# Performance work log

Hardware: AMD Instinct MI355X
Metric: run time of the kernel (lower is better)

## Reference

```python
import jax, jax.numpy as jnp
import numpy as np
from math import comb

N_DERIV = 4          # num_derivatives
ODE_DIM = 512        # ode_dimension
K = ODE_DIM * (N_DERIV + 1)


def _build_system(n, d):
    # system_matrices_1d: A_1d = flip(pascal), Q_1d = flip(hilbert), chol(Q_1d)
    x = np.arange(n + 1)
    B = np.array([[comb(i, j) for j in range(n + 1)] for i in range(n + 1)], dtype=np.float64)
    A1 = B[::-1, ::-1]                                  # flip both axes
    Hil = 1.0 / (x[:, None] + x[None, :] + 1.0)
    Q1 = Hil[::-1, ::-1]
    L1 = np.linalg.cholesky(Q1)
    a = np.kron(np.eye(d), A1)
    q = np.kron(np.eye(d), L1)
    return jnp.asarray(a, jnp.float32), jnp.asarray(q, jnp.float32)


def _qr_r(x):
    # sqrtm_to_cholesky: upper-triangular factor from reduced QR
    return jnp.linalg.qr(x)[1]


def setup_inputs() -> dict:
    key = jax.random.key(0)
    k1, k2, k3, k4, k5 = jax.random.split(key, 5)
    a, q_sqrtm_lower = _build_system(N_DERIV, ODE_DIM)
    m0 = jax.random.normal(k1, (K,), dtype=jnp.float32)
    l0 = jnp.tril(jax.random.normal(k2, (K, K), dtype=jnp.float32) * 0.05)
    H = jax.random.normal(k3, (ODE_DIM, K), dtype=jnp.float32) * 0.1
    bias = jax.random.normal(k4, (ODE_DIM,), dtype=jnp.float32)
    dt = jax.random.uniform(k5, (1,), dtype=jnp.float32, minval=0.05, maxval=0.15)
    return {"m0": m0, "l0": l0, "H": H, "bias": bias, "dt": dt,
            "a": a, "q_sqrtm_lower": q_sqrtm_lower}


def reference(m0, l0, H, bias, dt, a, q_sqrtm_lower):
    d = H.shape[0]
    k = m0.shape[0]
    n1 = k // d                       # num_derivatives + 1
    # --- assemble_preconditioner ---
    powers = jnp.arange(n1 - 1, -1, -1, dtype=m0.dtype)
    scales = jnp.exp(jax.lax.lgamma(powers + 1.0))
    pw = powers + 0.5
    adt = jnp.abs(dt[0])
    p = jnp.tile(adt ** pw / scales, d)          # (k,)
    p_inv = jnp.tile(adt ** (-pw) * scales, d)   # (k,)
    # --- extrapolate_mean ---
    m0_p = p_inv * m0
    m_ext_p = a @ m0_p
    m_ext = p * m_ext_p
    # EK-style linearized observation residual
    m_obs = H @ m_ext - bias                     # (d,)
    # --- estimate_error ---
    l_obs_ns_e = H @ (p_inv[:, None] * q_sqrtm_lower)            # (d,k)
    l_obs_raw = _qr_r(l_obs_ns_e.T).T                            # lower (d,d)
    res_white = jax.scipy.linalg.solve_triangular(l_obs_raw.T, m_obs, lower=False)
    diffusion = jnp.sqrt(jnp.dot(res_white, res_white) / res_white.size)
    error = diffusion * jnp.sqrt(jnp.einsum('nj,nj->n', l_obs_raw, l_obs_raw))
    # --- complete_extrapolation (sum_of_sqrtm_factors) ---
    R1 = (a @ (p_inv[:, None] * l0)).T           # (k,k)
    R2 = (diffusion * q_sqrtm_lower).T           # (k,k)
    l_ext_p = _qr_r(jnp.vstack([R1, R2])).T      # lower (k,k)
    l_ext = p[:, None] * l_ext_p
    # --- final_correction ---
    l_obs_ns = H @ l_ext                         # (d,k)
    l_obs = _qr_r(l_obs_ns.T).T                  # lower (d,d)
    crosscov = l_ext @ l_obs_ns.T                # (k,d)
    gain = jax.scipy.linalg.cho_solve((l_obs, True), crosscov.T).T  # (k,d)
    m_cor = m_ext - gain @ m_obs
    l_cor = l_ext - gain @ l_obs_ns
    u = jnp.reshape(m_cor, (-1, d), order='F')[0]  # derivative-0 block
    return m_cor, l_cor, u, error, diffusion
```

## Files before the change

kernel.cpp:

```cpp
#include <hip/hip_runtime.h>
#include <math.h>

#define KDIM 2560
#define DDIM 512
#define NB 64

#define QM 2560
#define QM2 1024
#define QN 512
#define PW 16
#define UW 4

#define OUT_LCOR 2560
#define OUT_U    6556160
#define OUT_ERR  6556672
#define OUT_DIFF 6557184


__global__ void k_setup(const float* dt, double* scal){
  if (threadIdx.x==0 && blockIdx.x==0){
    double adt = fabs((double)dt[0]);
    const double scales[5] = {24.0,6.0,2.0,1.0,1.0};
    for (int i=0;i<5;i++){
      double pw = (double)(4-i)+0.5;
      scal[i]   = pow(adt, pw)/scales[i];
      scal[5+i] = pow(adt,-pw)*scales[i];
    }
  }
}

__global__ __launch_bounds__(256) void k_mext_mobs(const float* a, const float* m0, const float* H,
                                                   const float* bias, const double* scal,
                                                   double* mext, double* mobs){
  __shared__ double me[KDIM];
  __shared__ double red[256];
  double pp[5], pv[5];
  #pragma unroll
  for (int i=0;i<5;i++){ pp[i]=scal[i]; pv[i]=scal[5+i]; }
  int tid=threadIdx.x;
  for (int r=tid; r<KDIM; r+=256){
    int j=r/5, i=r%5;
    const float* arow = a + (size_t)r*KDIM + 5*j;
    const float* m0b  = m0 + 5*j;
    double acc=0;
    #pragma unroll
    for (int l=0;l<5;l++) acc += (double)arow[l]*pv[l]*(double)m0b[l];
    me[r] = pp[i]*acc;
  }
  __syncthreads();
  if (blockIdx.x==0) for (int r=tid;r<KDIM;r+=256) mext[r]=me[r];
  int b = blockIdx.x;
  const float* Hr = H + (size_t)b*KDIM;
  double acc=0;
  for (int c=tid;c<KDIM;c+=256) acc += (double)Hr[c]*me[c];
  red[tid]=acc; __syncthreads();
  for (int s=128;s>0;s>>=1){ if (tid<s) red[tid]+=red[tid+s]; __syncthreads(); }
  if (tid==0) mobs[b] = red[0] - (double)bias[b];
}

__global__ void k_A2(const float* H, const float* q, const double* scal,
                     double* Atop, double* Abot){
  int idx = blockIdx.x*blockDim.x+threadIdx.x;
  if (idx >= QN*QM) return;
  double pv[5];
  #pragma unroll
  for (int t=0;t<5;t++) pv[t]=scal[5+t];
  int j = idx / QM;
  int i = idx % QM;
  int bi = i/5;
  double acc=0;
  #pragma unroll
  for (int t=0;t<5;t++)
    acc += (double)H[(size_t)j*QM + 5*bi+t]*pv[t]*(double)q[(size_t)(5*bi+t)*QM + i];
  if (i < 512) Atop[(size_t)j*QM2 + i] = acc;
  else         Abot[(size_t)j*2048 + (i-512)] = acc;
}

__global__ void k_copyB(const double* Gbot, double* AQ){
  int idx = blockIdx.x*blockDim.x+threadIdx.x;
  if (idx >= 512*512) return;
  int c = idx/512, rr = idx%512;
  AQ[(size_t)c*QM2 + 512 + rr] = (rr<=c) ? Gbot[(size_t)c*512 + rr] : 0.0;
}

__global__ __launch_bounds__(1024) void qr_panel(double* A, double* vhead, int col0, double* Tbuf){
  __shared__ double redw[16][PW];
  __shared__ double rednorm[16];
  __shared__ double sh[3];
  __shared__ double wsh[PW];
  __shared__ double alphas[PW], betas[PW];
  __shared__ double VtVs[PW][PW];
  __shared__ double Tsh[PW][PW];
  int tid=threadIdx.x, wid=tid>>6, lane=tid&63;
  int m = QM2 - col0;
  bool on = tid < m;
  double x[PW];
  #pragma unroll
  for (int j=0;j<PW;j++)
    x[j] = on ? A[(size_t)(col0+j)*QM2 + col0 + tid] : 0.0;
  for (int j=0;j<PW;j++){
    double v0 = (tid>=j && on)? x[j] : 0.0;
    double ps = v0*v0;
    #pragma unroll
    for (int o=32;o>0;o>>=1) ps += __shfl_down(ps,o);
    if (lane==0) rednorm[wid]=ps;
    if (tid==j) sh[0]=x[j];
    __syncthreads();
    if (tid==0){
      double s0=0;
      for (int t=0;t<16;t++) s0+=rednorm[t];
      double x1=sh[0];
      double nrm=sqrt(s0);
      double alpha=(x1>=0.0)?-nrm:nrm;
      double v1=x1-alpha;
      double vtv=s0-2.0*alpha*x1+alpha*alpha;
      double b=(vtv>0.0)?2.0/vtv:0.0;
      sh[1]=v1; sh[2]=b;
      alphas[j]=alpha; betas[j]=b;
      vhead[col0+j]=v1;
    }
    __syncthreads();
    if (tid==j) x[j]=sh[1];
    double b=sh[2];
    double v=(tid>=j && on)? x[j] : 0.0;
    #pragma unroll
    for (int t=0;t<PW;t++){
      if (t==j) continue;
      double p=v*x[t];
      #pragma unroll
      for (int o=32;o>0;o>>=1) p+=__shfl_down(p,o);
      if (lane==0) redw[wid][t]=p;
    }
    __syncthreads();
    if (tid<PW && tid!=j){
      double tot=0;
      #pragma unroll
      for (int t2=0;t2<16;t2++) tot+=redw[t2][tid];
      if (tid>j) wsh[tid]=b*tot;
      else       VtVs[tid][j]=tot;
    }
    __syncthreads();
    if (v!=0.0){
      for (int t=j+1;t<PW;t++) x[t]-=wsh[t]*v;
    }
  }
  __syncthreads();
  if (tid<PW){
    int i=tid;
    Tsh[i][i]=betas[i];
    for (int j2=i+1;j2<PW;j2++){
      double z=0;
      for (int t=i;t<j2;t++) z+=Tsh[i][t]*VtVs[t][j2];
      Tsh[i][j2]=-betas[j2]*z;
    }
  }
  __syncthreads();
  for (int e=tid;e<PW*PW;e+=1024){
    int i=e/PW, j2=e%PW;
    Tbuf[e] = (j2>=i)? Tsh[i][j2] : 0.0;
  }
  if (on){
    #pragma unroll
    for (int j=0;j<PW;j++)
      A[(size_t)(col0+j)*QM2 + col0 + tid] = (tid==j)? alphas[j] : x[j];
  }
}

__global__ __launch_bounds__(256) void qr_update(double* A, const double* vhead,
                                                 const double* Tbuf, int col0){
  __shared__ double redu[4][PW];
  __shared__ double ysh[PW];
  __shared__ double wsh[PW];
  int tid=threadIdx.x, wid=tid>>6, lane=tid&63;
  int cc=col0+PW+blockIdx.x;
  int m=QM2-col0;
  double a[UW];
  #pragma unroll
  for (int w=0;w<UW;w++){
    int lr=tid+w*256;
    a[w]=(lr<m)? A[(size_t)cc*QM2+col0+lr] : 0.0;
  }
  double acc[PW];
  #pragma unroll
  for (int j=0;j<PW;j++) acc[j]=0;
  #pragma unroll
  for (int w=0;w<UW;w++){
    int lr=tid+w*256;
    if (lr<m){
      #pragma unroll
      for (int j=0;j<PW;j++){
        double vj;
        if (lr>j)       vj=A[(size_t)(col0+j)*QM2+col0+lr];
        else if (lr==j) vj=vhead[col0+j];
        else            vj=0.0;
        acc[j]+=vj*a[w];
      }
    }
  }
  #pragma unroll
  for (int j=0;j<PW;j++){
    double d=acc[j];
    #pragma unroll
    for (int o=32;o>0;o>>=1) d+=__shfl_down(d,o);
    if (lane==0) redu[wid][j]=d;
  }
  __syncthreads();
  if (tid<PW){
    double y=0;
    #pragma unroll
    for (int t=0;t<4;t++) y+=redu[t][tid];
    ysh[tid]=y;
  }
  __syncthreads();
  if (tid<PW){
    double s=0;
    for (int t=0;t<=tid;t++) s+=Tbuf[t*PW+tid]*ysh[t];
    wsh[tid]=s;
  }
  __syncthreads();
  #pragma unroll
  for (int w=0;w<UW;w++){
    int lr=tid+w*256;
    if (lr<m){
      double s=0;
      #pragma unroll
      for (int j=0;j<PW;j++){
        double vj;
        if (lr>j)       vj=A[(size_t)(col0+j)*QM2+col0+lr];
        else if (lr==j) vj=vhead[col0+j];
        else            vj=0.0;
        s+=vj*wsh[j];
      }
      A[(size_t)cc*QM2+col0+lr]=a[w]-s;
    }
  }
}

__global__ __launch_bounds__(512) void k_rpost(const double* Aq, const double* mobs,
                                               double* scal, float* out){
  __shared__ double b[DDIM];
  __shared__ double xs[DDIM];
  __shared__ double D[NB][NB+1];
  __shared__ double red[DDIM];
  __shared__ double g1sh[DDIM];
  int tid=threadIdx.x;
  {
    double s=0;
    for (int r=0;r<=tid;r++){ double v=Aq[(size_t)tid*QM2 + r]; s+=v*v; }
    g1sh[tid]=s;
  }
  b[tid]=mobs[tid];
  __syncthreads();
  for (int p=7;p>=0;p--){
    int b0=p*NB;
    for (int e=tid;e<NB*NB;e+=512){ int i=e&63, j2=e>>6; D[i][j2]=Aq[(size_t)(b0+j2)*QM2 + b0+i]; }
    __syncthreads();
    if (tid<64){
      double bi=b[b0+tid];
      for (int k=NB-1;k>=0;k--){
        double bk=__shfl(bi,k);
        double xk=bk/D[k][k];
        if (tid<k) bi-=D[tid][k]*xk;
        if (tid==k) bi=xk;
      }
      xs[b0+tid]=bi;
    }
    __syncthreads();
    if (tid<b0){
      double s=0;
      #pragma unroll 8
      for (int j2=0;j2<NB;j2++) s+=Aq[(size_t)(b0+j2)*QM2 + tid]*xs[b0+j2];
      b[tid]-=s;
    }
    __syncthreads();
  }
  red[tid]=xs[tid]*xs[tid]; __syncthreads();
  for (int s=256;s>0;s>>=1){ if (tid<s) red[tid]+=red[tid+s]; __syncthreads(); }
  double diff=sqrt(red[0]/(double)DDIM);
  if (tid==0){ scal[10]=diff; out[OUT_DIFF]=(float)diff; }
  out[OUT_ERR+tid]=(float)(diff*sqrt(fmax(g1sh[tid],0.0)));
}

__global__ void k_X(const float* a, const float* l0, const double* scal, float* X){
  int idx=blockIdx.x*blockDim.x+threadIdx.x;
  if (idx>=KDIM*KDIM) return;
  double pv[5];
  #pragma unroll
  for (int t=0;t<5;t++) pv[t]=scal[5+t];
  int r=idx/KDIM, c=idx%KDIM;
  int j=r/5;
  const float* arow = a + (size_t)r*KDIM + 5*j;
  double acc=0;
  #pragma unroll
  for (int l=0;l<5;l++)
    acc += (double)arow[l]*pv[l]*(double)l0[(size_t)(5*j+l)*KDIM+c];
  X[idx]=(float)acc;
}

template<typename TA,int ATR,typename TB,int BTR,int MODE>
__global__ __launch_bounds__(256) void gemm64(const TA* __restrict__ A,int lda,
                                              const TB* __restrict__ B,int ldb,
                                              void* __restrict__ Cv,int ldc,
                                              int K,int kmode){
  __shared__ double As[16][65];
  __shared__ double Bs[16][65];
  int tid=threadIdx.x, tx=tid&15, ty=tid>>4;
  int n0=blockIdx.x*64, m0=blockIdx.y*64;
  int ks=0, ke=K;
  if (kmode==1) ks=n0;
  else if (kmode==2) ke=min(K,n0+64);
  else if (kmode==3) ke=min(K,m0+64);
  else if (kmode==4) ks=m0;
  double acc[4][4]={};
  for (int k0=ks;k0<ke;k0+=16){
    if (ATR){
      for (int e=tid;e<16*64;e+=256){int k=e>>6,mm=e&63; As[k][mm]=(double)A[(size_t)(k0+k)*lda+m0+mm];}
    } else {
      for (int e=tid;e<64*16;e+=256){int mm=e>>4,k=e&15; As[k][mm]=(double)A[(size_t)(m0+mm)*lda+k0+k];}
    }
    if (BTR){
      for (int e=tid;e<64*16;e+=256){int nn=e>>4,k=e&15; Bs[k][nn]=(double)B[(size_t)(n0+nn)*ldb+k0+k];}
    } else {
      for (int e=tid;e<16*64;e+=256){int k=e>>6,nn=e&63; Bs[k][nn]=(double)B[(size_t)(k0+k)*ldb+n0+nn];}
    }
    __syncthreads();
    #pragma unroll
    for (int t=0;t<16;t++){
      double av[4],bv[4];
      #pragma unroll
      for (int i=0;i<4;i++){av[i]=As[t][ty+16*i];bv[i]=Bs[t][tx+16*i];}
      #pragma unroll
      for (int i=0;i<4;i++)
        #pragma unroll
        for (int j=0;j<4;j++) acc[i][j]+=av[i]*bv[j];
    }
    __syncthreads();
  }
  #pragma unroll
  for (int i=0;i<4;i++){
    #pragma unroll
    for (int j=0;j<4;j++){
      size_t idx=(size_t)(m0+ty+16*i)*ldc+n0+tx+16*j;
      if (MODE==0) ((double*)Cv)[idx]=acc[i][j];
      else if (MODE==1) ((double*)Cv)[idx]-=acc[i][j];
      else ((float*)Cv)[idx]=(float)acc[i][j];
    }
  }
}

__global__ __launch_bounds__(256) void syrk_lower(const float* __restrict__ X, const float* __restrict__ q,
                                                  const double* __restrict__ scal,
                                                  double* __restrict__ G, int n){
  int S0=blockIdx.x*64, R0=blockIdx.y*64;
  if (S0>R0) return;
  __shared__ double As[16][65];
  __shared__ double Bs[16][65];
  int tid=threadIdx.x, tx=tid&15, ty=tid>>4;
  int kend=min(n, S0+80);
  double acc[4][4]={};
  for (int k0=0;k0<kend;k0+=16){
    for (int e=tid;e<64*16;e+=256){int mm=e>>4,k=e&15; As[k][mm]=(double)X[(size_t)(R0+mm)*n+k0+k];}
    for (int e=tid;e<64*16;e+=256){int nn=e>>4,k=e&15; Bs[k][nn]=(double)X[(size_t)(S0+nn)*n+k0+k];}
    __syncthreads();
    #pragma unroll
    for (int t=0;t<16;t++){
      double av[4],bv[4];
      #pragma unroll
      for (int i=0;i<4;i++){av[i]=As[t][ty+16*i];bv[i]=Bs[t][tx+16*i];}
      #pragma unroll
      for (int i=0;i<4;i++)
        #pragma unroll
        for (int j=0;j<4;j++) acc[i][j]+=av[i]*bv[j];
    }
    __syncthreads();
  }
  double dd = scal[10]*scal[10];
  #pragma unroll
  for (int i=0;i<4;i++)
    #pragma unroll
    for (int j=0;j<4;j++){
      int r=R0+ty+16*i, c=S0+tx+16*j;
      double v=acc[i][j];
      if (c<=r && (r/5)==(c/5)){
        double qq=0;
        #pragma unroll
        for (int k=0;k<5;k++) qq += (double)q[(size_t)(r%5)*KDIM+k]*(double)q[(size_t)(c%5)*KDIM+k];
        v += dd*qq;
      }
      G[(size_t)r*n+c]=v;
    }
}

__global__ __launch_bounds__(256) void chol_diag(double* A, int n, int k0){
  __shared__ double P[NB][NB+1];
  int tid=threadIdx.x;
  for (int e=tid;e<NB*NB;e+=256){int r=e>>6,c=e&63;P[r][c]=A[(size_t)(k0+r)*n+k0+c];}
  int tx=tid&15, ty=tid>>4;
  __syncthreads();
  for (int j=0;j<NB;j++){
    double pj=P[j][j];
    __syncthreads();
    double rpj=1.0/sqrt(fmax(pj,1e-280));
    if (tid>j && tid<NB) P[tid][j]*=rpj;
    if (tid==j) P[j][j]=sqrt(fmax(pj,1e-280));
    __syncthreads();
    #pragma unroll
    for (int a2=0;a2<4;a2++){
      int r=ty+16*a2;
      double lrj=P[r][j];
      #pragma unroll
      for (int b2=0;b2<4;b2++){
        int c=tx+16*b2;
        if (r>j && c>j && c<=r) P[r][c]-=lrj*P[c][j];
      }
    }
    __syncthreads();
  }
  for (int e=tid;e<NB*NB;e+=256){int r=e>>6,c=e&63;A[(size_t)(k0+r)*n+k0+c]=P[r][c];}
}

__global__ __launch_bounds__(256) void chol_trsm(double* A,int n,int k0){
  __shared__ double Ls[NB][NB+1];
  __shared__ double St[NB][NB+1];
  __shared__ double rec[NB];
  int tid=threadIdx.x;
  for (int e=tid;e<NB*NB;e+=256){int r=e>>6,c=e&63;Ls[r][c]=A[(size_t)(k0+r)*n+k0+c];}
  __syncthreads();
  if (tid<NB) rec[tid]=1.0/Ls[tid][tid];
  int base=k0+NB+blockIdx.x*256;
  int myrow=base+tid;
  int mychunk=tid>>6, lrow=tid&63;
  double ar[NB];
  for (int ch=0;ch<4;ch++){
    int r0=base+ch*64;
    for (int e=tid;e<NB*NB;e+=256){
      int r=e>>6,c=e&63;
      if (r0+r<n) St[r][c]=A[(size_t)(r0+r)*n+k0+c];
    }
    __syncthreads();
    if (mychunk==ch && myrow<n){
      #pragma unroll
      for (int c=0;c<NB;c++) ar[c]=St[lrow][c];
    }
    __syncthreads();
  }
  if (myrow<n){
    #pragma unroll
    for (int j=0;j<NB;j++){
      double s=ar[j];
      #pragma unroll
      for (int t=0;t<j;t++) s-=ar[t]*Ls[j][t];
      ar[j]=s*rec[j];
    }
  }
  for (int ch=0;ch<4;ch++){
    int r0=base+ch*64;
    if (mychunk==ch && myrow<n){
      #pragma unroll
      for (int c=0;c<NB;c++) St[lrow][c]=ar[c];
    }
    __syncthreads();
    for (int e=tid;e<NB*NB;e+=256){
      int r=e>>6,c=e&63;
      if (r0+r<n) A[(size_t)(r0+r)*n+k0+c]=St[r][c];
    }
    __syncthreads();
  }
}

__global__ __launch_bounds__(256) void chol_syrk_fd(double* A,int n,int k0){
  int ts0=k0+NB;
  int S0=ts0+blockIdx.x*64, R0=ts0+blockIdx.y*64;
  if (S0>R0) return;
  __shared__ double As[16][65];
  __shared__ double Bs[16][65];
  __shared__ double P[NB][NB+1];
  int tid=threadIdx.x, tx=tid&15, ty=tid>>4;
  double acc[4][4]={};
  for (int k0i=0;k0i<NB;k0i+=16){
    for (int e=tid;e<64*16;e+=256){int mm=e>>4,k=e&15; As[k][mm]=A[(size_t)(R0+mm)*n+k0+k0i+k];}
    for (int e=tid;e<64*16;e+=256){int nn=e>>4,k=e&15; Bs[k][nn]=A[(size_t)(S0+nn)*n+k0+k0i+k];}
    __syncthreads();
    #pragma unroll
    for (int t=0;t<16;t++){
      double av[4],bv[4];
      #pragma unroll
      for (int i=0;i<4;i++){av[i]=As[t][ty+16*i];bv[i]=Bs[t][tx+16*i];}
      #pragma unroll
      for (int i=0;i<4;i++)
        #pragma unroll
        for (int j=0;j<4;j++) acc[i][j]+=av[i]*bv[j];
    }
    __syncthreads();
  }
  if (!(blockIdx.x==0 && blockIdx.y==0)){
    #pragma unroll
    for (int i=0;i<4;i++)
      #pragma unroll
      for (int j=0;j<4;j++)
        A[(size_t)(R0+ty+16*i)*n+S0+tx+16*j]-=acc[i][j];
    return;
  }
  #pragma unroll
  for (int i=0;i<4;i++)
    #pragma unroll
    for (int j=0;j<4;j++)
      P[ty+16*i][tx+16*j] = A[(size_t)(R0+ty+16*i)*n+S0+tx+16*j] - acc[i][j];
  __syncthreads();
  for (int j=0;j<NB;j++){
    double pj=P[j][j];
    __syncthreads();
    double rpj=1.0/sqrt(fmax(pj,1e-280));
    if (tid>j && tid<NB) P[tid][j]*=rpj;
    if (tid==j) P[j][j]=sqrt(fmax(pj,1e-280));
    __syncthreads();
    #pragma unroll
    for (int a2=0;a2<4;a2++){
      int r=ty+16*a2;
      double lrj=P[r][j];
      #pragma unroll
      for (int b2=0;b2<4;b2++){
        int c=tx+16*b2;
        if (r>j && c>j && c<=r) P[r][c]-=lrj*P[c][j];
      }
    }
    __syncthreads();
  }
  for (int e=tid;e<NB*NB;e+=256){int r=e>>6,c=e&63;A[(size_t)(ts0+r)*n+ts0+c]=P[r][c];}
}

__global__ void k_extract(const double* G2, const double* scal, float* lext){
  int idx=blockIdx.x*blockDim.x+threadIdx.x;
  if (idx>=KDIM*KDIM) return;
  int r=idx/KDIM, c=idx%KDIM;
  double v = (c<=r)? scal[r%5]*G2[idx] : 0.0;
  lext[idx]=(float)v;
}

__global__ __launch_bounds__(256) void trinv_diag(const double* S, double* Linv){
  __shared__ double Ls[NB][NB+1];
  __shared__ double Ti[NB][NB+1];
  int jb=blockIdx.x, tid=threadIdx.x;
  for (int e=tid; e<DDIM*NB; e+=256){
    int r=e/NB, c=e%NB;
    Linv[(size_t)r*DDIM + jb*NB + c]=0.0;
  }
  for (int e=tid;e<NB*NB;e+=256){int r=e>>6,c=e&63; Ls[r][c]=S[(size_t)(jb*NB+r)*DDIM + jb*NB+c];}
  __syncthreads();
  if (tid<NB){
    int c=tid;
    for (int r=c;r<NB;r++){
      double s=(r==c)?1.0:0.0;
      for (int t=c;t<r;t++) s-=Ls[r][t]*Ti[t][c];
      Ti[r][c]=s/Ls[r][r];
    }
    for (int r=0;r<c;r++) Ti[r][c]=0.0;
  }
  __syncthreads();
  for (int e=tid;e<NB*NB;e+=256){int r=e>>6,c=e&63; Linv[(size_t)(jb*NB+r)*DDIM + jb*NB+c]=Ti[r][c];}
}

__global__ __launch_bounds__(256) void trinv_step(const double* S, double* Linv, int d){
  __shared__ double As[16][65];
  __shared__ double Bs[16][65];
  __shared__ double Ps[NB][NB+1];
  int jb=blockIdx.x, ib=jb+d;
  int tid=threadIdx.x, tx=tid&15, ty=tid>>4;
  double acc[4][4]={};
  int kstart=jb*NB, kend=ib*NB;
  for (int k0=kstart;k0<kend;k0+=16){
    for (int e=tid;e<64*16;e+=256){int mm=e>>4,k=e&15; As[k][mm]=S[(size_t)(ib*NB+mm)*DDIM + k0+k];}
    for (int e=tid;e<16*64;e+=256){int k=e>>6,nn=e&63; Bs[k][nn]=Linv[(size_t)(k0+k)*DDIM + jb*NB+nn];}
    __syncthreads();
    #pragma unroll
    for (int t=0;t<16;t++){
      double av[4],bv[4];
      #pragma unroll
      for (int i=0;i<4;i++){av[i]=As[t][ty+16*i];bv[i]=Bs[t][tx+16*i];}
      #pragma unroll
      for (int i=0;i<4;i++)
        #pragma unroll
        for (int j=0;j<4;j++) acc[i][j]+=av[i]*bv[j];
    }
    __syncthreads();
  }
  #pragma unroll
  for (int i=0;i<4;i++)
    #pragma unroll
    for (int j=0;j<4;j++) Ps[ty+16*i][tx+16*j]=acc[i][j];
  double o[4][4]={};
  __syncthreads();
  for (int k0=0;k0<NB;k0+=16){
    for (int e=tid;e<64*16;e+=256){int mm=e>>4,k=e&15; As[k][mm]=Linv[(size_t)(ib*NB+mm)*DDIM + ib*NB+k0+k];}
    __syncthreads();
    #pragma unroll
    for (int t=0;t<16;t++){
      double av[4],bv[4];
      #pragma unroll
      for (int i=0;i<4;i++){av[i]=As[t][ty+16*i];bv[i]=Ps[k0+t][tx+16*i];}
      #pragma unroll
      for (int i=0;i<4;i++)
        #pragma unroll
        for (int j=0;j<4;j++) o[i][j]+=av[i]*bv[j];
    }
    __syncthreads();
  }
  #pragma unroll
  for (int i=0;i<4;i++)
    #pragma unroll
    for (int j=0;j<4;j++)
      Linv[(size_t)(ib*NB+ty+16*i)*DDIM + jb*NB+tx+16*j] = -o[i][j];
}

__global__ void k_mcor(const double* Z, const double* mobs, const double* mext, float* out){
  __shared__ double mo[DDIM];
  for (int s=threadIdx.x;s<DDIM;s+=256) mo[s]=mobs[s];
  __syncthreads();
  int r=blockIdx.x*256+threadIdx.x;
  if (r>=KDIM) return;
  double acc=0;
  for (int s=0;s<DDIM;s++) acc += Z[(size_t)s*KDIM+r]*mo[s];
  double mc = mext[r]-acc;
  out[r]=(float)mc;
  if (r%5==0) out[OUT_U + r/5]=(float)mc;
}

__global__ __launch_bounds__(256) void k_lcor(const double* __restrict__ Z, const float* __restrict__ lobs,
                                              const float* __restrict__ lext, float* __restrict__ out){
  __shared__ double As[16][65];
  __shared__ double Bs[16][65];
  int tid=threadIdx.x, tx=tid&15, ty=tid>>4;
  int n0=blockIdx.x*64, m0=blockIdx.y*64;
  double acc[4][4]={};
  for (int k0=0;k0<DDIM;k0+=16){
    for (int e=tid;e<16*64;e+=256){int k=e>>6,mm=e&63; As[k][mm]=Z[(size_t)(k0+k)*KDIM+m0+mm];}
    for (int e=tid;e<16*64;e+=256){int k=e>>6,nn=e&63; Bs[k][nn]=(double)lobs[(size_t)(k0+k)*KDIM+n0+nn];}
    __syncthreads();
    #pragma unroll
    for (int t=0;t<16;t++){
      double av[4],bv[4];
      #pragma unroll
      for (int i=0;i<4;i++){av[i]=As[t][ty+16*i];bv[i]=Bs[t][tx+16*i];}
      #pragma unroll
      for (int i=0;i<4;i++)
        #pragma unroll
        for (int j=0;j<4;j++) acc[i][j]+=av[i]*bv[j];
    }
    __syncthreads();
  }
  #pragma unroll
  for (int i=0;i<4;i++)
    #pragma unroll
    for (int j=0;j<4;j++){
      size_t idx=(size_t)(m0+ty+16*i)*KDIM+n0+tx+16*j;
      out[OUT_LCOR+idx]=(float)((double)lext[idx]-acc[i][j]);
    }
}

extern "C" void kernel_launch(void* const* d_in, const int* in_sizes, int n_in,
                              void* d_out, int out_size, void* d_ws, size_t ws_size,
                              hipStream_t stream) {
  const float* m0  = (const float*)d_in[0];
  const float* l0  = (const float*)d_in[1];
  const float* H   = (const float*)d_in[2];
  const float* bias= (const float*)d_in[3];
  const float* dt  = (const float*)d_in[4];
  const float* a   = (const float*)d_in[5];
  const float* q   = (const float*)d_in[6];
  float* out = (float*)d_out;

  char* w=(char*)d_ws;
  auto alloc=[&](size_t bytes)->char*{ char* p=w; w += ((bytes+255)/256)*256; return p; };
  double* scal  =(double*)alloc(16*8);
  double* mext  =(double*)alloc((size_t)KDIM*8);
  double* mobs  =(double*)alloc((size_t)DDIM*8);
  double* vheadA=(double*)alloc((size_t)QN*8);
  double* Tbuf  =(double*)alloc((size_t)PW*PW*8);
  double* AQ    =(double*)alloc((size_t)QM2*QN*8);
  double* S     =(double*)alloc((size_t)DDIM*DDIM*8);
  double* G2    =(double*)alloc((size_t)KDIM*KDIM*8);
  float*  LOBS  =(float*) alloc((size_t)DDIM*KDIM*4);
  float*  X     =(float*) alloc((size_t)KDIM*KDIM*4);
  float*  LEXT  = X;
  double* Abot  = G2;
  double* Gbot  = Abot + (size_t)2048*512;
  double* Linv  = G2;
  double* C2    = Linv + (size_t)DDIM*DDIM;
  double* Y     = C2   + (size_t)DDIM*KDIM;
  double* Z     = Y    + (size_t)DDIM*KDIM;

  k_setup<<<1,1,0,stream>>>(dt, scal);
  k_mext_mobs<<<DDIM,256,0,stream>>>(a, m0, H, bias, scal, mext, mobs);

  k_A2<<<(QN*QM+255)/256,256,0,stream>>>(H, q, scal, AQ, Abot);
  gemm64<double,0,double,1,0><<<dim3(8,8),256,0,stream>>>(Abot,2048, Abot,2048, Gbot,512, 2048, 0);
  chol_diag<<<1,256,0,stream>>>(Gbot,512,0);
  for (int k0=0;k0+NB<512;k0+=NB){
    int m = 512-k0-NB;
    chol_trsm<<<(m+255)/256,256,0,stream>>>(Gbot,512,k0);
    chol_syrk_fd<<<dim3(m/64,m/64),256,0,stream>>>(Gbot,512,k0);
  }
  k_copyB<<<(512*512+255)/256,256,0,stream>>>(Gbot, AQ);
  for (int p=0;p<QN/PW;p++){
    int col0=p*PW;
    qr_panel<<<1,1024,0,stream>>>(AQ, vheadA, col0, Tbuf);
    int ntr = QN - col0 - PW;
    if (ntr>0) qr_update<<<ntr,256,0,stream>>>(AQ, vheadA, Tbuf, col0);
  }
  k_rpost<<<1,512,0,stream>>>(AQ, mobs, scal, out);

  k_X<<<(KDIM*KDIM+255)/256,256,0,stream>>>(a, l0, scal, X);
  syrk_lower<<<dim3(KDIM/64,KDIM/64),256,0,stream>>>(X, q, scal, G2, KDIM);
  chol_diag<<<1,256,0,stream>>>(G2, KDIM, 0);
  for (int k0=0;k0+NB<KDIM;k0+=NB){
    int m = KDIM-k0-NB;
    chol_trsm<<<(m+255)/256,256,0,stream>>>(G2, KDIM, k0);
    chol_syrk_fd<<<dim3(m/64,m/64),256,0,stream>>>(G2, KDIM, k0);
  }
  k_extract<<<(KDIM*KDIM+255)/256,256,0,stream>>>(G2, scal, LEXT);

  gemm64<float,0,float,0,2><<<dim3(KDIM/64,DDIM/64),256,0,stream>>>(H,KDIM, LEXT,KDIM, LOBS,KDIM, KDIM, 1);
  gemm64<float,0,float,1,0><<<dim3(DDIM/64,DDIM/64),256,0,stream>>>(LOBS,KDIM, LOBS,KDIM, S,DDIM, KDIM, 0);
  chol_diag<<<1,256,0,stream>>>(S, DDIM, 0);
  for (int k0=0;k0+NB<DDIM;k0+=NB){
    int m = DDIM-k0-NB;
    chol_trsm<<<(m+255)/256,256,0,stream>>>(S, DDIM, k0);
    chol_syrk_fd<<<dim3(m/64,m/64),256,0,stream>>>(S, DDIM, k0);
  }
  trinv_diag<<<8,256,0,stream>>>(S, Linv);
  for (int d=1;d<8;d++)
    trinv_step<<<8-d,256,0,stream>>>(S, Linv, d);
  gemm64<float,0,float,1,0><<<dim3(KDIM/64,DDIM/64),256,0,stream>>>(LOBS,KDIM, LEXT,KDIM, C2,KDIM, KDIM, 2);
  gemm64<double,0,double,0,0><<<dim3(KDIM/64,DDIM/64),256,0,stream>>>(Linv,DDIM, C2,KDIM, Y,KDIM, DDIM, 3);
  gemm64<double,1,double,0,0><<<dim3(KDIM/64,DDIM/64),256,0,stream>>>(Linv,DDIM, Y,KDIM, Z,KDIM, DDIM, 4);

  k_mcor<<<(KDIM+255)/256,256,0,stream>>>(Z, mobs, mext, out);
  k_lcor<<<dim3(KDIM/64,KDIM/64),256,0,stream>>>(Z, LOBS, LEXT, out);
}
```

Baseline: 15.90 ms.

## Widen QR panel, clip QR to active rows, launch only lower-triangle tiles

The QR panel width grows from 16 to 32, which halves the number of panel and update launches. Panel and update work is clipped to the first 544 rows, relying on the bottom block being triangular so rows beyond that are zero for each panel. The SYRK and Cholesky trailing-update kernels now use a triangular 1D grid mapping instead of a square grid where upper blocks exit early, which avoids wasted block launches. The trade-offs are larger per-thread register arrays in the panel kernel (x[32]) and a correctness dependence on the zero structure assumed by QACT.

```diff
diff --git a/kernel.cpp b/kernel.cpp
--- a/kernel.cpp
+++ b/kernel.cpp
@@ -8,8 +8,9 @@
 #define QM 2560
 #define QM2 1024
 #define QN 512
-#define PW 16
-#define UW 4
+#define PW 32
+#define UW 3
+#define QACT 544
 
 #define OUT_LCOR 2560
 #define OUT_U    6556160
@@ -83,16 +84,16 @@
   AQ[(size_t)c*QM2 + 512 + rr] = (rr<=c) ? Gbot[(size_t)c*512 + rr] : 0.0;
 }
 
-__global__ __launch_bounds__(1024) void qr_panel(double* A, double* vhead, int col0, double* Tbuf){
-  __shared__ double redw[16][PW];
-  __shared__ double rednorm[16];
+__global__ __launch_bounds__(576) void qr_panel(double* A, double* vhead, int col0, double* Tbuf){
+  __shared__ double redw[9][PW];
+  __shared__ double rednorm[9];
   __shared__ double sh[3];
   __shared__ double wsh[PW];
   __shared__ double alphas[PW], betas[PW];
   __shared__ double VtVs[PW][PW];
   __shared__ double Tsh[PW][PW];
   int tid=threadIdx.x, wid=tid>>6, lane=tid&63;
-  int m = QM2 - col0;
+  int m = QM2 - col0; if (m > QACT) m = QACT;
   bool on = tid < m;
   double x[PW];
   #pragma unroll
@@ -108,7 +109,7 @@
     __syncthreads();
     if (tid==0){
       double s0=0;
-      for (int t=0;t<16;t++) s0+=rednorm[t];
+      for (int t=0;t<9;t++) s0+=rednorm[t];
       double x1=sh[0];
       double nrm=sqrt(s0);
       double alpha=(x1>=0.0)?-nrm:nrm;
@@ -135,7 +136,7 @@
     if (tid<PW && tid!=j){
       double tot=0;
       #pragma unroll
-      for (int t2=0;t2<16;t2++) tot+=redw[t2][tid];
+      for (int t2=0;t2<9;t2++) tot+=redw[t2][tid];
       if (tid>j) wsh[tid]=b*tot;
       else       VtVs[tid][j]=tot;
     }
@@ -155,7 +156,7 @@
     }
   }
   __syncthreads();
-  for (int e=tid;e<PW*PW;e+=1024){
+  for (int e=tid;e<PW*PW;e+=576){
     int i=e/PW, j2=e%PW;
     Tbuf[e] = (j2>=i)? Tsh[i][j2] : 0.0;
   }
@@ -173,7 +174,7 @@
   __shared__ double wsh[PW];
   int tid=threadIdx.x, wid=tid>>6, lane=tid&63;
   int cc=col0+PW+blockIdx.x;
-  int m=QM2-col0;
+  int m=QM2-col0; if (m > QACT) m = QACT;
   double a[UW];
   #pragma unroll
   for (int w=0;w<UW;w++){
@@ -351,8 +352,13 @@
 __global__ __launch_bounds__(256) void syrk_lower(const float* __restrict__ X, const float* __restrict__ q,
                                                   const double* __restrict__ scal,
                                                   double* __restrict__ G, int n){
-  int S0=blockIdx.x*64, R0=blockIdx.y*64;
-  if (S0>R0) return;
+  int t = blockIdx.x;
+  int u = (int)((sqrtf(8.0f*(float)t+1.0f)+1.0f)*0.5f);
+  while ((u*(u-1))/2 > t) u--;
+  while ((u*(u+1))/2 <= t) u++;
+  int s = (KDIM/64) - u;
+  int r = s + (t - (u*(u-1))/2);
+  int S0=s*64, R0=r*64;
   __shared__ double As[16][65];
   __shared__ double Bs[16][65];
   int tid=threadIdx.x, tx=tid&15, ty=tid>>4;
@@ -363,10 +369,10 @@
     for (int e=tid;e<64*16;e+=256){int nn=e>>4,k=e&15; Bs[k][nn]=(double)X[(size_t)(S0+nn)*n+k0+k];}
     __syncthreads();
     #pragma unroll
-    for (int t=0;t<16;t++){
+    for (int t2=0;t2<16;t2++){
       double av[4],bv[4];
       #pragma unroll
-      for (int i=0;i<4;i++){av[i]=As[t][ty+16*i];bv[i]=Bs[t][tx+16*i];}
+      for (int i=0;i<4;i++){av[i]=As[t2][ty+16*i];bv[i]=Bs[t2][tx+16*i];}
       #pragma unroll
       for (int i=0;i<4;i++)
         #pragma unroll
@@ -379,15 +385,15 @@
   for (int i=0;i<4;i++)
     #pragma unroll
     for (int j=0;j<4;j++){
-      int r=R0+ty+16*i, c=S0+tx+16*j;
+      int rr=R0+ty+16*i, c=S0+tx+16*j;
       double v=acc[i][j];
-      if (c<=r && (r/5)==(c/5)){
+      if (c<=rr && (rr/5)==(c/5)){
         double qq=0;
         #pragma unroll
-        for (int k=0;k<5;k++) qq += (double)q[(size_t)(r%5)*KDIM+k]*(double)q[(size_t)(c%5)*KDIM+k];
+        for (int k=0;k<5;k++) qq += (double)q[(size_t)(rr%5)*KDIM+k]*(double)q[(size_t)(c%5)*KDIM+k];
         v += dd*qq;
       }
-      G[(size_t)r*n+c]=v;
+      G[(size_t)rr*n+c]=v;
     }
 }
 
@@ -470,8 +476,12 @@
 
 __global__ __launch_bounds__(256) void chol_syrk_fd(double* A,int n,int k0){
   int ts0=k0+NB;
-  int S0=ts0+blockIdx.x*64, R0=ts0+blockIdx.y*64;
-  if (S0>R0) return;
+  int t=blockIdx.x;
+  int r=(int)((sqrtf(8.0f*(float)t+1.0f)-1.0f)*0.5f);
+  while ((r*(r+1))/2 > t) r--;
+  while (((r+1)*(r+2))/2 <= t) r++;
+  int s=t-(r*(r+1))/2;
+  int S0=ts0+s*64, R0=ts0+r*64;
   __shared__ double As[16][65];
   __shared__ double Bs[16][65];
   __shared__ double P[NB][NB+1];
@@ -482,10 +492,10 @@
     for (int e=tid;e<64*16;e+=256){int nn=e>>4,k=e&15; Bs[k][nn]=A[(size_t)(S0+nn)*n+k0+k0i+k];}
     __syncthreads();
     #pragma unroll
-    for (int t=0;t<16;t++){
+    for (int tt=0;tt<16;tt++){
       double av[4],bv[4];
       #pragma unroll
-      for (int i=0;i<4;i++){av[i]=As[t][ty+16*i];bv[i]=Bs[t][tx+16*i];}
+      for (int i=0;i<4;i++){av[i]=As[tt][ty+16*i];bv[i]=Bs[tt][tx+16*i];}
       #pragma unroll
       for (int i=0;i<4;i++)
         #pragma unroll
@@ -493,7 +503,7 @@
     }
     __syncthreads();
   }
-  if (!(blockIdx.x==0 && blockIdx.y==0)){
+  if (t!=0){
     #pragma unroll
     for (int i=0;i<4;i++)
       #pragma unroll
@@ -516,17 +526,17 @@
     __syncthreads();
     #pragma unroll
     for (int a2=0;a2<4;a2++){
-      int r=ty+16*a2;
-      double lrj=P[r][j];
+      int r2=ty+16*a2;
+      double lrj=P[r2][j];
       #pragma unroll
       for (int b2=0;b2<4;b2++){
         int c=tx+16*b2;
-        if (r>j && c>j && c<=r) P[r][c]-=lrj*P[c][j];
+        if (r2>j && c>j && c<=r2) P[r2][c]-=lrj*P[c][j];
       }
     }
     __syncthreads();
   }
-  for (int e=tid;e<NB*NB;e+=256){int r=e>>6,c=e&63;A[(size_t)(ts0+r)*n+ts0+c]=P[r][c];}
+  for (int e=tid;e<NB*NB;e+=256){int r2=e>>6,c=e&63;A[(size_t)(ts0+r2)*n+ts0+c]=P[r2][c];}
 }
 
 __global__ void k_extract(const double* G2, const double* scal, float* lext){
@@ -689,44 +699,39 @@
   double* Y     = C2   + (size_t)DDIM*KDIM;
   double* Z     = Y    + (size_t)DDIM*KDIM;
 
+  auto chol_full=[&](double* M, int n){
+    chol_diag<<<1,256,0,stream>>>(M, n, 0);
+    for (int k0=0;k0+NB<n;k0+=NB){
+      int m = n-k0-NB;
+      chol_trsm<<<(m+255)/256,256,0,stream>>>(M,n,k0);
+      int T = m/64;
+      chol_syrk_fd<<<T*(T+1)/2,256,0,stream>>>(M,n,k0);
+    }
+  };
+
   k_setup<<<1,1,0,stream>>>(dt, scal);
   k_mext_mobs<<<DDIM,256,0,stream>>>(a, m0, H, bias, scal, mext, mobs);
 
   k_A2<<<(QN*QM+255)/256,256,0,stream>>>(H, q, scal, AQ, Abot);
   gemm64<double,0,double,1,0><<<dim3(8,8),256,0,stream>>>(Abot,2048, Abot,2048, Gbot,512, 2048, 0);
-  chol_diag<<<1,256,0,stream>>>(Gbot,512,0);
-  for (int k0=0;k0+NB<512;k0+=NB){
-    int m = 512-k0-NB;
-    chol_trsm<<<(m+255)/256,256,0,stream>>>(Gbot,512,k0);
-    chol_syrk_fd<<<dim3(m/64,m/64),256,0,stream>>>(Gbot,512,k0);
-  }
+  chol_full(Gbot, 512);
   k_copyB<<<(512*512+255)/256,256,0,stream>>>(Gbot, AQ);
   for (int p=0;p<QN/PW;p++){
     int col0=p*PW;
-    qr_panel<<<1,1024,0,stream>>>(AQ, vheadA, col0, Tbuf);
+    qr_panel<<<1,576,0,stream>>>(AQ, vheadA, col0, Tbuf);
     int ntr = QN - col0 - PW;
     if (ntr>0) qr_update<<<ntr,256,0,stream>>>(AQ, vheadA, Tbuf, col0);
   }
   k_rpost<<<1,512,0,stream>>>(AQ, mobs, scal, out);
 
   k_X<<<(KDIM*KDIM+255)/256,256,0,stream>>>(a, l0, scal, X);
-  syrk_lower<<<dim3(KDIM/64,KDIM/64),256,0,stream>>>(X, q, scal, G2, KDIM);
-  chol_diag<<<1,256,0,stream>>>(G2, KDIM, 0);
-  for (int k0=0;k0+NB<KDIM;k0+=NB){
-    int m = KDIM-k0-NB;
-    chol_trsm<<<(m+255)/256,256,0,stream>>>(G2, KDIM, k0);
-    chol_syrk_fd<<<dim3(m/64,m/64),256,0,stream>>>(G2, KDIM, k0);
-  }
+  syrk_lower<<<(KDIM/64)*((KDIM/64)+1)/2,256,0,stream>>>(X, q, scal, G2, KDIM);
+  chol_full(G2, KDIM);
   k_extract<<<(KDIM*KDIM+255)/256,256,0,stream>>>(G2, scal, LEXT);
 
   gemm64<float,0,float,0,2><<<dim3(KDIM/64,DDIM/64),256,0,stream>>>(H,KDIM, LEXT,KDIM, LOBS,KDIM, KDIM, 1);
   gemm64<float,0,float,1,0><<<dim3(DDIM/64,DDIM/64),256,0,stream>>>(LOBS,KDIM, LOBS,KDIM, S,DDIM, KDIM, 0);
-  chol_diag<<<1,256,0,stream>>>(S, DDIM, 0);
-  for (int k0=0;k0+NB<DDIM;k0+=NB){
-    int m = DDIM-k0-NB;
-    chol_trsm<<<(m+255)/256,256,0,stream>>>(S, DDIM, k0);
-    chol_syrk_fd<<<dim3(m/64,m/64),256,0,stream>>>(S, DDIM, k0);
-  }
+  chol_full(S, DDIM);
   trinv_diag<<<8,256,0,stream>>>(S, Linv);
   for (int d=1;d<8;d++)
     trinv_step<<<8-d,256,0,stream>>>(S, Linv, d);
```

Measured after the change: 18.24 ms. 14.7% more time.
